# Performance work log

Hardware: AMD Instinct MI355X
Metric: run time of the kernel (lower is better)

The kernel has to match this reference:

```python
import jax, jax.numpy as jnp
import numpy as np

N_HEAD = 16

def setup_inputs() -> dict:
    key = jax.random.key(0)
    ks = jax.random.split(key, 5)
    d = 1024
    x = jax.random.normal(ks[0], (2, 2048, d), dtype=jnp.float32)
    Wqkv = jax.random.normal(ks[1], (d, 3 * d), dtype=jnp.float32) * (1.0 / np.sqrt(d))
    bqkv = jnp.zeros((3 * d,), dtype=jnp.float32)
    Wproj = jax.random.normal(ks[2], (d, d), dtype=jnp.float32) * (1.0 / np.sqrt(d))
    bproj = jnp.zeros((d,), dtype=jnp.float32)
    return {"x": x, "Wqkv": Wqkv, "bqkv": bqkv, "Wproj": Wproj, "bproj": bproj}


def reference(x, Wqkv, bqkv, Wproj, bproj):
    B, T, C = x.shape
    H = N_HEAD
    Dh = C // H
    qkv = x @ Wqkv + bqkv                      # [B, T, 3C]
    q, k, v = jnp.split(qkv, 3, axis=-1)
    # [B, T, C] -> [B, H, T, Dh]
    q = q.reshape(B, T, H, Dh).transpose(0, 2, 1, 3)
    k = k.reshape(B, T, H, Dh).transpose(0, 2, 1, 3)
    v = v.reshape(B, T, H, Dh).transpose(0, 2, 1, 3)
    scale = 1.0 / np.sqrt(Dh)
    att = jnp.einsum('bhqd,bhkd->bhqk', q, k) * scale
    causal = jnp.tril(jnp.ones((T, T), dtype=bool))
    att = jnp.where(causal[None, None, :, :], att, jnp.float32(-jnp.inf))
    att = jax.nn.softmax(att, axis=-1)
    y = jnp.einsum('bhqk,bhkd->bhqd', att, v)  # [B, H, T, Dh]
    y = y.transpose(0, 2, 1, 3).reshape(B, T, C)
    return y @ Wproj + bproj
```

## Files before the change

kernel.cpp:

```cpp
#include <hip/hip_runtime.h>
#include <math.h>


typedef __attribute__((ext_vector_type(8))) short short8;
typedef __attribute__((ext_vector_type(4))) short short4v;
typedef __attribute__((ext_vector_type(4))) float floatx4;
typedef __attribute__((ext_vector_type(16))) float floatx16;
typedef __attribute__((ext_vector_type(2))) unsigned int uint2v;
typedef __attribute__((ext_vector_type(4))) unsigned int uint4v;

__device__ __forceinline__ unsigned short f2bf(float f) {
  unsigned u = __float_as_uint(f);
  return (unsigned short)((u + 0x7fff + ((u >> 16) & 1)) >> 16);
}

__device__ __forceinline__ unsigned cvtpk(float a, float b) {
  unsigned r;
  asm("v_cvt_pk_bf16_f32 %0, %1, %2" : "=v"(r) : "v"(a), "v"(b));
  return r;
}

__device__ __forceinline__ short8 mk8(unsigned w0, unsigned w1, unsigned w2,
                                      unsigned w3) {
  uint4v v = {w0, w1, w2, w3};
  return __builtin_bit_cast(short8, v);
}

__device__ __forceinline__ void gld16(const unsigned short* g, unsigned short* l) {
  __builtin_amdgcn_global_load_lds(
      (const __attribute__((address_space(1))) unsigned int*)g,
      (__attribute__((address_space(3))) unsigned int*)l, 16, 0, 0);
}

__device__ __forceinline__ void vmcnt4() {
  asm volatile("s_waitcnt vmcnt(4)" ::: "memory");
}
__device__ __forceinline__ void vmcnt0() {
  asm volatile("s_waitcnt vmcnt(0)" ::: "memory");
}

__device__ __forceinline__ void pack_a_body(const float* __restrict__ in,
                                            unsigned short* __restrict__ out,
                                            int K, int m0, int k0,
                                            unsigned short (*lds)[72], int t) {
  {
    int ml = t >> 2, kl = (t & 3) * 16;
    const float4* p = (const float4*)(in + (size_t)(m0 + ml) * K + k0 + kl);
    unsigned short* q = &lds[ml][kl];
#pragma unroll
    for (int c = 0; c < 4; ++c) {
      float4 v = p[c];
      q[c * 4 + 0] = f2bf(v.x);
      q[c * 4 + 1] = f2bf(v.y);
      q[c * 4 + 2] = f2bf(v.z);
      q[c * 4 + 3] = f2bf(v.w);
    }
  }
  __syncthreads();
  int chunk = t >> 3, sub = t & 7;
  int mt = chunk >> 3, kc = chunk & 7;
  unsigned short tmp[16];
#pragma unroll
  for (int j2 = 0; j2 < 2; ++j2)
#pragma unroll
    for (int j = 0; j < 8; ++j)
      tmp[j2 * 8 + j] = lds[mt * 16 + sub * 2 + j2][kc * 8 + j];
  size_t ofs = ((size_t)(m0 >> 4) + mt) * (16 * (size_t)K) +
               ((size_t)(k0 >> 3) + kc) * 128 + sub * 16;
  *(int4*)(out + ofs) = *(int4*)(tmp);
  *(int4*)(out + ofs + 8) = *(int4*)(tmp + 8);
}

__device__ __forceinline__ void pack_bt_body(const float* __restrict__ in,
                                             unsigned short* __restrict__ out,
                                             int K, int N, int n0, int k0,
                                             unsigned short (*lds)[72], int t) {
  {
    int kl = t >> 2, nl = (t & 3) * 16;
    const float4* p = (const float4*)(in + (size_t)(k0 + kl) * N + n0 + nl);
#pragma unroll
    for (int c = 0; c < 4; ++c) {
      float4 v = p[c];
      lds[nl + c * 4 + 0][kl] = f2bf(v.x);
      lds[nl + c * 4 + 1][kl] = f2bf(v.y);
      lds[nl + c * 4 + 2][kl] = f2bf(v.z);
      lds[nl + c * 4 + 3][kl] = f2bf(v.w);
    }
  }
  __syncthreads();
  int chunk = t >> 3, sub = t & 7;
  int nt = chunk >> 3, kc = chunk & 7;
  unsigned short tmp[16];
#pragma unroll
  for (int j2 = 0; j2 < 2; ++j2)
#pragma unroll
    for (int j = 0; j < 8; ++j)
      tmp[j2 * 8 + j] = lds[nt * 16 + sub * 2 + j2][kc * 8 + j];
  size_t ofs = ((size_t)(n0 >> 4) + nt) * (16 * (size_t)K) +
               ((size_t)(k0 >> 3) + kc) * 128 + sub * 16;
  *(int4*)(out + ofs) = *(int4*)(tmp);
  *(int4*)(out + ofs + 8) = *(int4*)(tmp + 8);
}

__global__ __launch_bounds__(256) void pack_all(
    const float* __restrict__ x, const float* __restrict__ Wqkv,
    const float* __restrict__ Wproj, unsigned short* __restrict__ xbf,
    unsigned short* __restrict__ wqkvF, unsigned short* __restrict__ wprojF) {
  __shared__ __align__(16) unsigned short lds[64][72];
  const int b = blockIdx.x, t = threadIdx.x;
  if (b < 1024) {
    pack_a_body(x, xbf, 1024, (b >> 4) * 64, (b & 15) * 64, lds, t);
  } else if (b < 1792) {
    int b2 = b - 1024;
    pack_bt_body(Wqkv, wqkvF, 1024, 3072, (b2 % 48) * 64, (b2 / 48) * 64, lds, t);
  } else {
    int b3 = b - 1792;
    pack_bt_body(Wproj, wprojF, 1024, 1024, (b3 & 15) * 64, (b3 >> 4) * 64, lds, t);
  }
}

template <int MODE>
__global__ __launch_bounds__(256, 3) void gemm_lds(
    const unsigned short* __restrict__ A, const unsigned short* __restrict__ B,
    const float* __restrict__ bias, float* __restrict__ Cout,
    unsigned short* __restrict__ Qb, unsigned short* __restrict__ Kb,
    unsigned short* __restrict__ Vt, int M, int N, int K) {
  const int tid = threadIdx.x;
  const int wave = tid >> 6, lane = tid & 63;
  const int quad = lane >> 4, l15 = lane & 15;
  const int wr = wave >> 1, wc = wave & 1;

  const int nbn = N >> 7;
  const int colsPerX = nbn >> 3;
  const int xcd = (int)(blockIdx.x & 7);
  const int idx = (int)(blockIdx.x >> 3);
  const int bn = xcd * colsPerX + (colsPerX == 1 ? 0 : (idx % colsPerX));
  const int bm = (colsPerX == 1) ? idx : (idx / colsPerX);

  const int mt0 = bm * 8;
  const int nt0 = bn * 8;

  __shared__ __align__(16) unsigned short As[8192];
  __shared__ __align__(16) unsigned short Bs[8192];

  const unsigned short* spA[4];
  const unsigned short* spB[4];
#pragma unroll
  for (int j = 0; j < 4; ++j) {
    int c = wave * 4 + j;
    spA[j] = A + ((size_t)(mt0 + (c >> 1))) * (16 * (size_t)K) +
             (c & 1) * 512 + lane * 8;
    spB[j] = B + ((size_t)(nt0 + (c >> 1))) * (16 * (size_t)K) +
             (c & 1) * 512 + lane * 8;
  }

  floatx4 acc[4][4];
#pragma unroll
  for (int i = 0; i < 4; ++i)
#pragma unroll
    for (int j = 0; j < 4; ++j) acc[i][j] = (floatx4)0.0f;

  const int fofs = quad * 128 + l15 * 8;
  const int nk = K >> 6;

  for (int kk = 0; kk < nk; ++kk) {
#pragma unroll
    for (int j = 0; j < 4; ++j) {
      gld16(spA[j], &As[(wave * 4 + j) * 512]);
      gld16(spB[j], &Bs[(wave * 4 + j) * 512]);
      spA[j] += 1024;
      spB[j] += 1024;
    }
    __syncthreads();

#pragma unroll
    for (int ks = 0; ks < 2; ++ks) {
      short8 fa[4], fb[4];
#pragma unroll
      for (int im = 0; im < 4; ++im)
        fa[im] = *(const short8*)&As[((wr * 4 + im) * 2 + ks) * 512 + fofs];
#pragma unroll
      for (int in = 0; in < 4; ++in)
        fb[in] = *(const short8*)&Bs[((wc * 4 + in) * 2 + ks) * 512 + fofs];
#pragma unroll
      for (int im = 0; im < 4; ++im)
#pragma unroll
        for (int in = 0; in < 4; ++in)
          acc[im][in] = __builtin_amdgcn_mfma_f32_16x16x32_bf16(
              fa[im], fb[in], acc[im][in], 0, 0, 0);
    }
    if (kk + 1 < nk) __syncthreads();
  }

  const int m0w = bm * 128 + wr * 64;
  const int n0w = bn * 128 + wc * 64;

  if (MODE == 0) {
    const float QSCALE = 0.18033688f;
#pragma unroll
    for (int im = 0; im < 4; ++im) {
      int mbase = m0w + im * 16 + quad * 4;
      int bb = mbase >> 11, tb = mbase & 2047;
#pragma unroll
      for (int in = 0; in < 4; ++in) {
        int n = n0w + in * 16 + l15;
        float bv = bias[n];
        int which = n >> 10;
        int h = (n >> 6) & 15;
        int d = n & 63;
        size_t bh_ = (size_t)(bb * 16 + h);
        if (which == 2) {
          size_t base = bh_ * 131072 + (size_t)(d >> 5) * 65536 +
                        (size_t)(tb >> 4) * 512 +
                        (size_t)((d & 31) + 32 * ((tb & 15) >> 3)) * 8 +
                        (tb & 7);
          short4v pk;
#pragma unroll
          for (int r = 0; r < 4; ++r) pk[r] = (short)f2bf(acc[im][in][r] + bv);
          *(short4v*)(Vt + base) = pk;
        } else {
          size_t base = bh_ * 131072 + (size_t)(tb >> 5) * 2048 +
                        (size_t)(d >> 4) * 512 +
                        (size_t)((tb & 31) + 32 * ((d & 15) >> 3)) * 8 +
                        (d & 7);
          if (which == 0) {
#pragma unroll
            for (int r = 0; r < 4; ++r)
              Qb[base + r * 8] = f2bf((acc[im][in][r] + bv) * QSCALE);
          } else {
#pragma unroll
            for (int r = 0; r < 4; ++r)
              Kb[base + r * 8] = f2bf(acc[im][in][r] + bv);
          }
        }
      }
    }
  } else {
#pragma unroll
    for (int im = 0; im < 4; ++im) {
      int mbase = m0w + im * 16 + quad * 4;
#pragma unroll
      for (int in = 0; in < 4; ++in) {
        int n = n0w + in * 16 + l15;
        float bv = bias[n];
#pragma unroll
        for (int r = 0; r < 4; ++r)
          Cout[(size_t)(mbase + r) * N + n] = acc[im][in][r] + bv;
      }
    }
  }
}

__device__ __forceinline__ void pack_swap(const floatx16& s, short8& lo,
                                          short8& hi) {
  unsigned P0 = cvtpk(s[0], s[1]), P1 = cvtpk(s[2], s[3]);
  unsigned P2 = cvtpk(s[4], s[5]), P3 = cvtpk(s[6], s[7]);
  unsigned P4 = cvtpk(s[8], s[9]), P5 = cvtpk(s[10], s[11]);
  unsigned P6 = cvtpk(s[12], s[13]), P7 = cvtpk(s[14], s[15]);
  uint2v a = __builtin_amdgcn_permlane32_swap(P0, P2, false, false);
  uint2v b = __builtin_amdgcn_permlane32_swap(P1, P3, false, false);
  uint2v c = __builtin_amdgcn_permlane32_swap(P4, P6, false, false);
  uint2v d = __builtin_amdgcn_permlane32_swap(P5, P7, false, false);
  lo = mk8(a.x, b.x, a.y, b.y);
  hi = mk8(c.x, d.x, c.y, d.y);
}

__global__ __launch_bounds__(256, 2) void attn_mfma(
    const unsigned short* __restrict__ Q, const unsigned short* __restrict__ K,
    const unsigned short* __restrict__ Vt, unsigned short* __restrict__ Y) {
  const int b = (int)blockIdx.x;
  const int xcd = b & 7, qi = b >> 3;
  const int bh = xcd * 4 + (qi & 3);
  const int m = 15 - (qi >> 2);
  const int wave = threadIdx.x >> 6;
  const int lane = threadIdx.x & 63;
  const int j = m * 4 + wave;
  const int t0 = j * 32;
  const int l31 = lane & 31, h = lane >> 5;
  const int lofs8 = lane * 8;

  __shared__ __align__(16) unsigned short KV[2][8192];

  const unsigned short* Qb = Q + (size_t)bh * 131072;
  const unsigned short* Kb = K + (size_t)bh * 131072;
  const unsigned short* Vb = Vt + (size_t)bh * 131072;

  auto stage = [&](int buf, int jtN) {
    unsigned short* l = &KV[buf][wave * 2048];
    const unsigned short* g =
        (wave < 2) ? (Kb + (size_t)jtN * 4096 + wave * 2048)
                   : (Vb + (size_t)(wave & 1) * 65536 + (size_t)jtN * 2048);
    g += lofs8;
#pragma unroll
    for (int i = 0; i < 4; ++i) gld16(g + i * 512, l + i * 512);
  };

  short8 qf[4];
#pragma unroll
  for (int c = 0; c < 4; ++c)
    qf[c] = *(const short8*)(Qb + (size_t)j * 2048 + c * 512 + lofs8);

  floatx16 o0 = (floatx16)0.0f, o1 = (floatx16)0.0f;
  float lp[4] = {0.f, 0.f, 0.f, 0.f};

  const int ntiles = (j >> 1) + 1;
  const int ntB = 2 * m + 2;

  stage(0, 0);
  int cur = 0;

  for (int jt = 0; jt < ntB; ++jt) {
    if (jt + 1 < ntB) {
      stage(cur ^ 1, jt + 1);
      vmcnt4();
    } else {
      vmcnt0();
    }
    __builtin_amdgcn_s_barrier();
    __builtin_amdgcn_sched_barrier(0);

    const unsigned short* Lb = KV[cur];
    short8 kf0[4], kf1[4];
#pragma unroll
    for (int c = 0; c < 4; ++c) {
      kf0[c] = *(const short8*)&Lb[c * 512 + lofs8];
      kf1[c] = *(const short8*)&Lb[2048 + c * 512 + lofs8];
    }

    floatx16 sa0 = (floatx16)0.0f, sa1 = (floatx16)0.0f;
#pragma unroll
    for (int c = 0; c < 4; ++c) {
      sa0 = __builtin_amdgcn_mfma_f32_32x32x16_bf16(kf0[c], qf[c], sa0, 0, 0, 0);
      sa1 = __builtin_amdgcn_mfma_f32_32x32x16_bf16(kf1[c], qf[c], sa1, 0, 0, 0);
    }

    if (jt >= ntiles - 1) {
#pragma unroll
      for (int r = 0; r < 16; ++r) {
        int row = (r & 3) + 8 * (r >> 2) + 4 * h;
        int key = jt * 64 + row;
        if (key > t0 + l31) sa0[r] = -__builtin_inff();
        if (key + 32 > t0 + l31) sa1[r] = -__builtin_inff();
      }
    }

#pragma unroll
    for (int r = 0; r < 16; ++r) {
      float p0 = exp2f(sa0[r]);
      float p1 = exp2f(sa1[r]);
      sa0[r] = p0;
      sa1[r] = p1;
      lp[r & 3] += p0 + p1;
    }

    short8 pb0, pb1, pb2, pb3;
    pack_swap(sa0, pb0, pb1);
    pack_swap(sa1, pb2, pb3);

    short8 vf0[4], vf1[4];
#pragma unroll
    for (int kc = 0; kc < 4; ++kc) {
      vf0[kc] = *(const short8*)&Lb[4096 + kc * 512 + lofs8];
      vf1[kc] = *(const short8*)&Lb[6144 + kc * 512 + lofs8];
    }

    o0 = __builtin_amdgcn_mfma_f32_32x32x16_bf16(vf0[0], pb0, o0, 0, 0, 0);
    o1 = __builtin_amdgcn_mfma_f32_32x32x16_bf16(vf1[0], pb0, o1, 0, 0, 0);
    o0 = __builtin_amdgcn_mfma_f32_32x32x16_bf16(vf0[1], pb1, o0, 0, 0, 0);
    o1 = __builtin_amdgcn_mfma_f32_32x32x16_bf16(vf1[1], pb1, o1, 0, 0, 0);
    o0 = __builtin_amdgcn_mfma_f32_32x32x16_bf16(vf0[2], pb2, o0, 0, 0, 0);
    o1 = __builtin_amdgcn_mfma_f32_32x32x16_bf16(vf1[2], pb2, o1, 0, 0, 0);
    o0 = __builtin_amdgcn_mfma_f32_32x32x16_bf16(vf0[3], pb3, o0, 0, 0, 0);
    o1 = __builtin_amdgcn_mfma_f32_32x32x16_bf16(vf1[3], pb3, o1, 0, 0, 0);

    __builtin_amdgcn_sched_barrier(0);
    __builtin_amdgcn_s_barrier();
    cur ^= 1;
  }

  float l_acc = (lp[0] + lp[1]) + (lp[2] + lp[3]);
  l_acc += __shfl_xor(l_acc, 32);
  const float inv = 1.0f / l_acc;

  const int b_ = bh >> 4, hh = bh & 15;
  const int mglob = b_ * 2048 + t0 + l31;
  const size_t mofs = (size_t)(mglob >> 4) * 16384 + (size_t)(mglob & 15) * 8;
#pragma unroll
  for (int db = 0; db < 2; ++db) {
    const floatx16& o = db ? o1 : o0;
#pragma unroll
    for (int g = 0; g < 4; ++g) {
      int d0 = db * 32 + 8 * g + 4 * h;
      int kf0 = hh * 64 + d0;
      size_t ofs = mofs + (size_t)(kf0 >> 3) * 128 + (kf0 & 7);
      short4v pk;
#pragma unroll
      for (int r = 0; r < 4; ++r) pk[r] = (short)f2bf(o[4 * g + r] * inv);
      *(short4v*)(Y + ofs) = pk;
    }
  }
}

extern "C" void kernel_launch(void* const* d_in, const int* in_sizes, int n_in,
                              void* d_out, int out_size, void* d_ws,
                              size_t ws_size, hipStream_t stream) {
  const float* x = (const float*)d_in[0];
  const float* Wqkv = (const float*)d_in[1];
  const float* bqkv = (const float*)d_in[2];
  const float* Wproj = (const float*)d_in[3];
  const float* bproj = (const float*)d_in[4];
  float* out = (float*)d_out;

  const int C = 1024;
  const int M = 4096;

  char* ws = (char*)d_ws;
  unsigned short* qbuf = (unsigned short*)ws;
  unsigned short* kbuf = (unsigned short*)(ws + 8388608);
  unsigned short* vtbuf = (unsigned short*)(ws + 16777216);
  unsigned short* ybuf = (unsigned short*)(ws + 25165824);
  unsigned short* xbf = (unsigned short*)(ws + 33554432);
  unsigned short* wqkvF = (unsigned short*)(ws + 41943040);
  unsigned short* wprojF = (unsigned short*)(ws + 48234496);

  dim3 blk(256);
  pack_all<<<dim3(2048), blk, 0, stream>>>(x, Wqkv, Wproj, xbf, wqkvF, wprojF);
  gemm_lds<0><<<dim3((M / 128) * (3 * C / 128)), blk, 0, stream>>>(
      xbf, wqkvF, bqkv, nullptr, qbuf, kbuf, vtbuf, M, 3 * C, C);
  attn_mfma<<<dim3(512), blk, 0, stream>>>(qbuf, kbuf, vtbuf, ybuf);
  gemm_lds<1><<<dim3((M / 128) * (C / 128)), blk, 0, stream>>>(
      ybuf, wprojF, bproj, out, nullptr, nullptr, nullptr, M, C, C);
}
```

Baseline: 178.7 us.

## Double-buffer GEMM K-loop and split attention KV range across waves with LDS merge

The GEMM now uses two LDS buffers with K-step 32 and prefetches the next tile while computing the current one, with vmcnt waits replacing full syncthreads. The attention kernel drops LDS staging. Each block pairs a short and a long query row (p and 63-p) for load balance, and two waves split each row's key range, reading K/V straight from global memory into registers. The partial O and l values are merged through LDS before writeback. The launch doubles to 1024 blocks, which adds parallelism and balance at the cost of more global traffic without LDS sharing of K/V.

```diff
diff --git a/kernel.cpp b/kernel.cpp
--- a/kernel.cpp
+++ b/kernel.cpp
@@ -140,18 +140,15 @@
   const int mt0 = bm * 8;
   const int nt0 = bn * 8;
 
-  __shared__ __align__(16) unsigned short As[8192];
-  __shared__ __align__(16) unsigned short Bs[8192];
-
-  const unsigned short* spA[4];
-  const unsigned short* spB[4];
-#pragma unroll
-  for (int j = 0; j < 4; ++j) {
-    int c = wave * 4 + j;
-    spA[j] = A + ((size_t)(mt0 + (c >> 1))) * (16 * (size_t)K) +
-             (c & 1) * 512 + lane * 8;
-    spB[j] = B + ((size_t)(nt0 + (c >> 1))) * (16 * (size_t)K) +
-             (c & 1) * 512 + lane * 8;
+  __shared__ __align__(16) unsigned short As[2][4096];
+  __shared__ __align__(16) unsigned short Bs[2][4096];
+
+  const unsigned short* spA[2];
+  const unsigned short* spB[2];
+#pragma unroll
+  for (int jj = 0; jj < 2; ++jj) {
+    spA[jj] = A + ((size_t)(mt0 + wave * 2 + jj)) * (16 * (size_t)K) + lane * 8;
+    spB[jj] = B + ((size_t)(nt0 + wave * 2 + jj)) * (16 * (size_t)K) + lane * 8;
   }
 
   floatx4 acc[4][4];
@@ -161,35 +158,56 @@
     for (int j = 0; j < 4; ++j) acc[i][j] = (floatx4)0.0f;
 
   const int fofs = quad * 128 + l15 * 8;
-  const int nk = K >> 6;
+  const int nk = K >> 5;
+
+#pragma unroll
+  for (int jj = 0; jj < 2; ++jj) {
+    gld16(spA[jj], &As[0][(wave * 2 + jj) * 512]);
+    gld16(spB[jj], &Bs[0][(wave * 2 + jj) * 512]);
+    spA[jj] += 512;
+    spB[jj] += 512;
+  }
+#pragma unroll
+  for (int jj = 0; jj < 2; ++jj) {
+    gld16(spA[jj], &As[1][(wave * 2 + jj) * 512]);
+    gld16(spB[jj], &Bs[1][(wave * 2 + jj) * 512]);
+    spA[jj] += 512;
+    spB[jj] += 512;
+  }
 
   for (int kk = 0; kk < nk; ++kk) {
-#pragma unroll
-    for (int j = 0; j < 4; ++j) {
-      gld16(spA[j], &As[(wave * 4 + j) * 512]);
-      gld16(spB[j], &Bs[(wave * 4 + j) * 512]);
-      spA[j] += 1024;
-      spB[j] += 1024;
-    }
-    __syncthreads();
-
-#pragma unroll
-    for (int ks = 0; ks < 2; ++ks) {
-      short8 fa[4], fb[4];
-#pragma unroll
-      for (int im = 0; im < 4; ++im)
-        fa[im] = *(const short8*)&As[((wr * 4 + im) * 2 + ks) * 512 + fofs];
+    if (kk + 1 < nk) vmcnt4(); else vmcnt0();
+    __builtin_amdgcn_s_barrier();
+    __builtin_amdgcn_sched_barrier(0);
+
+    const unsigned short* Ab = As[kk & 1];
+    const unsigned short* Bb = Bs[kk & 1];
+    short8 fa[4], fb[4];
+#pragma unroll
+    for (int im = 0; im < 4; ++im)
+      fa[im] = *(const short8*)&Ab[(wr * 4 + im) * 512 + fofs];
+#pragma unroll
+    for (int in = 0; in < 4; ++in)
+      fb[in] = *(const short8*)&Bb[(wc * 4 + in) * 512 + fofs];
+#pragma unroll
+    for (int im = 0; im < 4; ++im)
 #pragma unroll
       for (int in = 0; in < 4; ++in)
-        fb[in] = *(const short8*)&Bs[((wc * 4 + in) * 2 + ks) * 512 + fofs];
-#pragma unroll
-      for (int im = 0; im < 4; ++im)
-#pragma unroll
-        for (int in = 0; in < 4; ++in)
-          acc[im][in] = __builtin_amdgcn_mfma_f32_16x16x32_bf16(
-              fa[im], fb[in], acc[im][in], 0, 0, 0);
-    }
-    if (kk + 1 < nk) __syncthreads();
+        acc[im][in] = __builtin_amdgcn_mfma_f32_16x16x32_bf16(
+            fa[im], fb[in], acc[im][in], 0, 0, 0);
+
+    __builtin_amdgcn_sched_barrier(0);
+    __builtin_amdgcn_s_barrier();
+
+    if (kk + 2 < nk) {
+#pragma unroll
+      for (int jj = 0; jj < 2; ++jj) {
+        gld16(spA[jj], &As[kk & 1][(wave * 2 + jj) * 512]);
+        gld16(spB[jj], &Bs[kk & 1][(wave * 2 + jj) * 512]);
+        spA[jj] += 512;
+        spB[jj] += 512;
+      }
+    }
   }
 
   const int m0w = bm * 128 + wr * 64;
@@ -269,32 +287,27 @@
     const unsigned short* __restrict__ Q, const unsigned short* __restrict__ K,
     const unsigned short* __restrict__ Vt, unsigned short* __restrict__ Y) {
   const int b = (int)blockIdx.x;
-  const int xcd = b & 7, qi = b >> 3;
-  const int bh = xcd * 4 + (qi & 3);
-  const int m = 15 - (qi >> 2);
+  const int xcd = b & 7;
+  const int bh = xcd * 4 + ((b >> 3) & 3);
+  const int p = b >> 5;
   const int wave = threadIdx.x >> 6;
   const int lane = threadIdx.x & 63;
-  const int j = m * 4 + wave;
-  const int t0 = j * 32;
   const int l31 = lane & 31, h = lane >> 5;
   const int lofs8 = lane * 8;
 
-  __shared__ __align__(16) unsigned short KV[2][8192];
+  const int sel = wave >> 1;
+  const int j = sel ? p : (63 - p);
+  const int Tj = (j >> 1) + 1;
+  const int halfT = (Tj + 1) >> 1;
+  const int seg = wave & 1;
+  const int ta = seg ? halfT : 0;
+  const int tb = seg ? Tj : halfT;
+  const int t0 = j * 32;
 
   const unsigned short* Qb = Q + (size_t)bh * 131072;
   const unsigned short* Kb = K + (size_t)bh * 131072;
   const unsigned short* Vb = Vt + (size_t)bh * 131072;
 
-  auto stage = [&](int buf, int jtN) {
-    unsigned short* l = &KV[buf][wave * 2048];
-    const unsigned short* g =
-        (wave < 2) ? (Kb + (size_t)jtN * 4096 + wave * 2048)
-                   : (Vb + (size_t)(wave & 1) * 65536 + (size_t)jtN * 2048);
-    g += lofs8;
-#pragma unroll
-    for (int i = 0; i < 4; ++i) gld16(g + i * 512, l + i * 512);
-  };
-
   short8 qf[4];
 #pragma unroll
   for (int c = 0; c < 4; ++c)
@@ -303,100 +316,114 @@
   floatx16 o0 = (floatx16)0.0f, o1 = (floatx16)0.0f;
   float lp[4] = {0.f, 0.f, 0.f, 0.f};
 
-  const int ntiles = (j >> 1) + 1;
-  const int ntB = 2 * m + 2;
-
-  stage(0, 0);
-  int cur = 0;
-
-  for (int jt = 0; jt < ntB; ++jt) {
-    if (jt + 1 < ntB) {
-      stage(cur ^ 1, jt + 1);
-      vmcnt4();
-    } else {
-      vmcnt0();
-    }
-    __builtin_amdgcn_s_barrier();
-    __builtin_amdgcn_sched_barrier(0);
-
-    const unsigned short* Lb = KV[cur];
+  if (ta < tb) {
     short8 kf0[4], kf1[4];
 #pragma unroll
     for (int c = 0; c < 4; ++c) {
-      kf0[c] = *(const short8*)&Lb[c * 512 + lofs8];
-      kf1[c] = *(const short8*)&Lb[2048 + c * 512 + lofs8];
-    }
-
-    floatx16 sa0 = (floatx16)0.0f, sa1 = (floatx16)0.0f;
-#pragma unroll
-    for (int c = 0; c < 4; ++c) {
-      sa0 = __builtin_amdgcn_mfma_f32_32x32x16_bf16(kf0[c], qf[c], sa0, 0, 0, 0);
-      sa1 = __builtin_amdgcn_mfma_f32_32x32x16_bf16(kf1[c], qf[c], sa1, 0, 0, 0);
-    }
-
-    if (jt >= ntiles - 1) {
+      kf0[c] = *(const short8*)(Kb + (size_t)(2 * ta) * 2048 + c * 512 + lofs8);
+      kf1[c] =
+          *(const short8*)(Kb + (size_t)(2 * ta + 1) * 2048 + c * 512 + lofs8);
+    }
+
+    for (int jt = ta; jt < tb; ++jt) {
+      short8 vf0[4], vf1[4];
+#pragma unroll
+      for (int kc = 0; kc < 4; ++kc) {
+        vf0[kc] = *(const short8*)(Vb + (size_t)(4 * jt + kc) * 512 + lofs8);
+        vf1[kc] =
+            *(const short8*)(Vb + 65536 + (size_t)(4 * jt + kc) * 512 + lofs8);
+      }
+
+      floatx16 sa0 = (floatx16)0.0f, sa1 = (floatx16)0.0f;
+#pragma unroll
+      for (int c = 0; c < 4; ++c) {
+        sa0 = __builtin_amdgcn_mfma_f32_32x32x16_bf16(kf0[c], qf[c], sa0, 0, 0, 0);
+        sa1 = __builtin_amdgcn_mfma_f32_32x32x16_bf16(kf1[c], qf[c], sa1, 0, 0, 0);
+      }
+
+      if (jt + 1 < tb) {
+#pragma unroll
+        for (int c = 0; c < 4; ++c) {
+          kf0[c] = *(const short8*)(Kb + (size_t)(2 * jt + 2) * 2048 + c * 512 +
+                                    lofs8);
+          kf1[c] = *(const short8*)(Kb + (size_t)(2 * jt + 3) * 2048 + c * 512 +
+                                    lofs8);
+        }
+      }
+
+      if (jt == Tj - 1) {
+#pragma unroll
+        for (int r = 0; r < 16; ++r) {
+          int row = (r & 3) + 8 * (r >> 2) + 4 * h;
+          int key = jt * 64 + row;
+          if (key > t0 + l31) sa0[r] = -__builtin_inff();
+          if (key + 32 > t0 + l31) sa1[r] = -__builtin_inff();
+        }
+      }
+
 #pragma unroll
       for (int r = 0; r < 16; ++r) {
-        int row = (r & 3) + 8 * (r >> 2) + 4 * h;
-        int key = jt * 64 + row;
-        if (key > t0 + l31) sa0[r] = -__builtin_inff();
-        if (key + 32 > t0 + l31) sa1[r] = -__builtin_inff();
-      }
-    }
-
-#pragma unroll
-    for (int r = 0; r < 16; ++r) {
-      float p0 = exp2f(sa0[r]);
-      float p1 = exp2f(sa1[r]);
-      sa0[r] = p0;
-      sa1[r] = p1;
-      lp[r & 3] += p0 + p1;
-    }
-
-    short8 pb0, pb1, pb2, pb3;
-    pack_swap(sa0, pb0, pb1);
-    pack_swap(sa1, pb2, pb3);
-
-    short8 vf0[4], vf1[4];
-#pragma unroll
-    for (int kc = 0; kc < 4; ++kc) {
-      vf0[kc] = *(const short8*)&Lb[4096 + kc * 512 + lofs8];
-      vf1[kc] = *(const short8*)&Lb[6144 + kc * 512 + lofs8];
-    }
-
-    o0 = __builtin_amdgcn_mfma_f32_32x32x16_bf16(vf0[0], pb0, o0, 0, 0, 0);
-    o1 = __builtin_amdgcn_mfma_f32_32x32x16_bf16(vf1[0], pb0, o1, 0, 0, 0);
-    o0 = __builtin_amdgcn_mfma_f32_32x32x16_bf16(vf0[1], pb1, o0, 0, 0, 0);
-    o1 = __builtin_amdgcn_mfma_f32_32x32x16_bf16(vf1[1], pb1, o1, 0, 0, 0);
-    o0 = __builtin_amdgcn_mfma_f32_32x32x16_bf16(vf0[2], pb2, o0, 0, 0, 0);
-    o1 = __builtin_amdgcn_mfma_f32_32x32x16_bf16(vf1[2], pb2, o1, 0, 0, 0);
-    o0 = __builtin_amdgcn_mfma_f32_32x32x16_bf16(vf0[3], pb3, o0, 0, 0, 0);
-    o1 = __builtin_amdgcn_mfma_f32_32x32x16_bf16(vf1[3], pb3, o1, 0, 0, 0);
-
-    __builtin_amdgcn_sched_barrier(0);
-    __builtin_amdgcn_s_barrier();
-    cur ^= 1;
+        float p0 = exp2f(sa0[r]);
+        float p1 = exp2f(sa1[r]);
+        sa0[r] = p0;
+        sa1[r] = p1;
+        lp[r & 3] += p0 + p1;
+      }
+
+      short8 pb0, pb1, pb2, pb3;
+      pack_swap(sa0, pb0, pb1);
+      pack_swap(sa1, pb2, pb3);
+
+      o0 = __builtin_amdgcn_mfma_f32_32x32x16_bf16(vf0[0], pb0, o0, 0, 0, 0);
+      o1 = __builtin_amdgcn_mfma_f32_32x32x16_bf16(vf1[0], pb0, o1, 0, 0, 0);
+      o0 = __builtin_amdgcn_mfma_f32_32x32x16_bf16(vf0[1], pb1, o0, 0, 0, 0);
+      o1 = __builtin_amdgcn_mfma_f32_32x32x16_bf16(vf1[1], pb1, o1, 0, 0, 0);
+      o0 = __builtin_amdgcn_mfma_f32_32x32x16_bf16(vf0[2], pb2, o0, 0, 0, 0);
+      o1 = __builtin_amdgcn_mfma_f32_32x32x16_bf16(vf1[2], pb2, o1, 0, 0, 0);
+      o0 = __builtin_amdgcn_mfma_f32_32x32x16_bf16(vf0[3], pb3, o0, 0, 0, 0);
+      o1 = __builtin_amdgcn_mfma_f32_32x32x16_bf16(vf1[3], pb3, o1, 0, 0, 0);
+    }
   }
 
   float l_acc = (lp[0] + lp[1]) + (lp[2] + lp[3]);
   l_acc += __shfl_xor(l_acc, 32);
-  const float inv = 1.0f / l_acc;
-
-  const int b_ = bh >> 4, hh = bh & 15;
-  const int mglob = b_ * 2048 + t0 + l31;
-  const size_t mofs = (size_t)(mglob >> 4) * 16384 + (size_t)(mglob & 15) * 8;
-#pragma unroll
-  for (int db = 0; db < 2; ++db) {
-    const floatx16& o = db ? o1 : o0;
-#pragma unroll
-    for (int g = 0; g < 4; ++g) {
-      int d0 = db * 32 + 8 * g + 4 * h;
-      int kf0 = hh * 64 + d0;
-      size_t ofs = mofs + (size_t)(kf0 >> 3) * 128 + (kf0 & 7);
-      short4v pk;
-#pragma unroll
-      for (int r = 0; r < 4; ++r) pk[r] = (short)f2bf(o[4 * g + r] * inv);
-      *(short4v*)(Y + ofs) = pk;
+
+  __shared__ float OM[2][32][64];
+  __shared__ float LM[2][64];
+  if (seg) {
+#pragma unroll
+    for (int r = 0; r < 16; ++r) {
+      OM[sel][r][lane] = o0[r];
+      OM[sel][16 + r][lane] = o1[r];
+    }
+    LM[sel][lane] = l_acc;
+  }
+  __syncthreads();
+  if (!seg) {
+#pragma unroll
+    for (int r = 0; r < 16; ++r) {
+      o0[r] += OM[sel][r][lane];
+      o1[r] += OM[sel][16 + r][lane];
+    }
+    l_acc += LM[sel][lane];
+    const float inv = 1.0f / l_acc;
+
+    const int b_ = bh >> 4, hh = bh & 15;
+    const int mglob = b_ * 2048 + t0 + l31;
+    const size_t mofs = (size_t)(mglob >> 4) * 16384 + (size_t)(mglob & 15) * 8;
+#pragma unroll
+    for (int db = 0; db < 2; ++db) {
+      const floatx16& o = db ? o1 : o0;
+#pragma unroll
+      for (int g = 0; g < 4; ++g) {
+        int d0 = db * 32 + 8 * g + 4 * h;
+        int kf0 = hh * 64 + d0;
+        size_t ofs = mofs + (size_t)(kf0 >> 3) * 128 + (kf0 & 7);
+        short4v pk;
+#pragma unroll
+        for (int r = 0; r < 4; ++r) pk[r] = (short)f2bf(o[4 * g + r] * inv);
+        *(short4v*)(Y + ofs) = pk;
+      }
     }
   }
 }
@@ -427,7 +454,7 @@
   pack_all<<<dim3(2048), blk, 0, stream>>>(x, Wqkv, Wproj, xbf, wqkvF, wprojF);
   gemm_lds<0><<<dim3((M / 128) * (3 * C / 128)), blk, 0, stream>>>(
       xbf, wqkvF, bqkv, nullptr, qbuf, kbuf, vtbuf, M, 3 * C, C);
-  attn_mfma<<<dim3(512), blk, 0, stream>>>(qbuf, kbuf, vtbuf, ybuf);
+  attn_mfma<<<dim3(1024), blk, 0, stream>>>(qbuf, kbuf, vtbuf, ybuf);
   gemm_lds<1><<<dim3((M / 128) * (C / 128)), blk, 0, stream>>>(
       ybuf, wprojF, bproj, out, nullptr, nullptr, nullptr, M, C, C);
 }
```

After: 179.9 us. Within noise of the previous version (+0.7%).
